# Kernel optimization log

Hardware: AMD Instinct MI355X
Metric: run time of the kernel (lower is better)

Reference implementation:

```python
import jax, jax.numpy as jnp
import numpy as np

D_MODEL = 768
D_STATE = 64
HEADDIM = 64
CHUNK = 64
EXPAND = 2
D_CONV = 4
D_INNER = EXPAND * D_MODEL          # 1536
NHEADS = D_INNER // HEADDIM         # 24
CONV_CH = D_INNER + 2 * D_STATE     # 1664
D_IN_PROJ = 2 * D_INNER + 2 * D_STATE + NHEADS  # 3224
EPS = 1e-5


def segsum(x):
    # x: (..., T) -> (..., T, T); entry [i, j] = sum_{k=j+1..i} x[k] for i>=j, -inf above diag
    T = x.shape[-1]
    cs = jnp.cumsum(x, axis=-1)
    seg = cs[..., :, None] - cs[..., None, :]
    mask = jnp.tril(jnp.ones((T, T), dtype=bool))
    return jnp.where(mask, seg, -jnp.inf)


def ssd(x, A, B, C, chunk):
    # x: (b, L, h, p), A: (b, L, h), B/C: (b, L, n)
    b, L, h, p = x.shape
    nc = L // chunk
    x = x.reshape(b, nc, chunk, h, p)
    A = A.reshape(b, nc, chunk, h).transpose(0, 3, 1, 2)   # (b, h, nc, l)
    B = B.reshape(b, nc, chunk, -1)
    C = C.reshape(b, nc, chunk, -1)
    A_cs = jnp.cumsum(A, axis=-1)                          # (b, h, nc, l)
    Lm = jnp.exp(segsum(A))                                # (b, h, nc, l, s)
    # intra-chunk (diagonal) term
    Y_diag = jnp.einsum('bcln,bcsn,bhcls,bcshp->bclhp', C, B, Lm, x)
    # per-chunk states
    decay_states = jnp.exp(A_cs[..., -1:] - A_cs)          # (b, h, nc, l)
    states = jnp.einsum('bcln,bhcl,bclhp->bchpn', B, decay_states, x)
    states = jnp.concatenate([jnp.zeros_like(states[:, :1]), states], axis=1)
    # inter-chunk recurrence via segsum over chunk totals
    chunk_sums = jnp.pad(A_cs[..., -1], ((0, 0), (0, 0), (1, 0)))
    decay_chunk = jnp.exp(segsum(chunk_sums))              # (b, h, nc+1, nc+1)
    new_states = jnp.einsum('bhzc,bchpn->bzhpn', decay_chunk, states)
    states = new_states[:, :-1]                            # (b, nc, h, p, n)
    Y_off = jnp.einsum('bcln,bchpn,bhcl->bclhp', C, states, jnp.exp(A_cs))
    return (Y_diag + Y_off).reshape(b, L, h, p)


def setup_inputs() -> dict:
    key = jax.random.key(0)
    ks = jax.random.split(key, 6)
    b, L = 2, 4096
    u = jax.random.normal(ks[0], (b, L, D_MODEL), dtype=jnp.float32)
    W_in = jax.random.normal(ks[1], (D_IN_PROJ, D_MODEL), dtype=jnp.float32) * (D_MODEL ** -0.5)
    conv_w = jax.random.normal(ks[2], (CONV_CH, 1, D_CONV), dtype=jnp.float32) * 0.3
    conv_b = jnp.zeros((CONV_CH,), dtype=jnp.float32)
    dt_bias = jnp.zeros((NHEADS,), dtype=jnp.float32)
    A_log = jax.random.normal(ks[3], (NHEADS,), dtype=jnp.float32) * 0.1
    D = jnp.ones((NHEADS,), dtype=jnp.float32)
    norm_w = jnp.ones((D_INNER,), dtype=jnp.float32)
    W_out = jax.random.normal(ks[4], (D_MODEL, D_INNER), dtype=jnp.float32) * (D_INNER ** -0.5)
    return {'u': u, 'W_in': W_in, 'conv_w': conv_w, 'conv_b': conv_b,
            'dt_bias': dt_bias, 'A_log': A_log, 'D': D, 'norm_w': norm_w, 'W_out': W_out}


def reference(u, W_in, conv_w, conv_b, dt_bias, A_log, D, norm_w, W_out):
    b, L, _ = u.shape
    zxbcdt = u @ W_in.T                                    # (b, L, d_in_proj)
    z = zxbcdt[..., :D_INNER]
    xBC = zxbcdt[..., D_INNER:D_INNER + CONV_CH]
    dt = jax.nn.softplus(zxbcdt[..., -NHEADS:] + dt_bias)  # (b, L, h)
    # causal depthwise conv (left pad d_conv-1, matches torch pad+slice)
    xBC = jax.lax.conv_general_dilated(
        xBC.transpose(0, 2, 1), conv_w, (1,), [(D_CONV - 1, 0)],
        dimension_numbers=('NCH', 'OIH', 'NCH'), feature_group_count=CONV_CH)
    xBC = jax.nn.silu(xBC.transpose(0, 2, 1) + conv_b)
    x = xBC[..., :D_INNER].reshape(b, L, NHEADS, HEADDIM)
    Bm = xBC[..., D_INNER:D_INNER + D_STATE]
    Cm = xBC[..., -D_STATE:]
    A = -jnp.exp(A_log)                                    # (h,)
    y = ssd(x * dt[..., None], A * dt, Bm, Cm, CHUNK)
    y = y + x * D[None, None, :, None]
    y = y.reshape(b, L, D_INNER)
    # gated RMSNorm
    y = y * jax.nn.silu(z)
    y = y * jax.lax.rsqrt(jnp.mean(y * y, axis=-1, keepdims=True) + EPS) * norm_w
    return y @ W_out.T
```

## Files before the change

### kernel.cpp

```cpp
#include <hip/hip_runtime.h>

typedef __attribute__((ext_vector_type(4))) float f4;
typedef __attribute__((ext_vector_type(8))) short bfx8;
typedef __attribute__((ext_vector_type(4))) float f32x4;
typedef __attribute__((ext_vector_type(4))) unsigned int u32x4;
typedef __attribute__((ext_vector_type(4))) unsigned short u16x4;
typedef __attribute__((ext_vector_type(8))) unsigned short u16x8;
typedef unsigned short ushort_t;

#define DM 768
#define DINNER 1536
#define NH 24
#define XBCW 1664
#define DINPROJ 3224
#define NPAD1 3328
#define NCHUNK 64
#define BROWS 8192
#define PADB 72

__device__ inline ushort_t f2bf(float f) {
    unsigned u = __builtin_bit_cast(unsigned, f);
    unsigned r = (u + 0x7FFF + ((u >> 16) & 1)) >> 16;
    return (ushort_t)r;
}
__device__ inline float bf2f(ushort_t u) {
    return __builtin_bit_cast(float, (unsigned)u << 16);
}
__device__ inline u32x4 pack8(f4 a, f4 b) {
    u32x4 o;
    o[0] = (unsigned)f2bf(a[0]) | ((unsigned)f2bf(a[1]) << 16);
    o[1] = (unsigned)f2bf(a[2]) | ((unsigned)f2bf(a[3]) << 16);
    o[2] = (unsigned)f2bf(b[0]) | ((unsigned)f2bf(b[1]) << 16);
    o[3] = (unsigned)f2bf(b[2]) | ((unsigned)f2bf(b[3]) << 16);
    return o;
}
__device__ inline void gl16(const void* g, void* l) {
    __builtin_amdgcn_global_load_lds((const __attribute__((address_space(1))) void*)g,
                                     (__attribute__((address_space(3))) void*)l, 16, 0, 0);
}

__global__ __launch_bounds__(256) void fill_kernel(float* out, int n, float v) {
    int i = blockIdx.x * 256 + threadIdx.x;
    if (i < n) out[i] = v;
}

__global__ __launch_bounds__(256) void cvt_kernel(const float* __restrict__ in,
                                                  ushort_t* __restrict__ outp, long n4) {
    long i = (long)blockIdx.x * 256 + threadIdx.x;
    if (i >= n4) return;
    f4 v = *(const f4*)&in[i * 4];
    u16x4 o;
    o[0] = f2bf(v[0]); o[1] = f2bf(v[1]); o[2] = f2bf(v[2]); o[3] = f2bf(v[3]);
    *(u16x4*)&outp[i * 4] = o;
}

__global__ __launch_bounds__(256) void cvt_pad_kernel(const float* __restrict__ in,
                                                      ushort_t* __restrict__ outp) {
    long q = (long)blockIdx.x * 256 + threadIdx.x;
    if (q >= (long)NPAD1 * 192) return;
    int row = (int)(q / 192);
    int cq = (int)(q % 192);
    u16x4 o = {0, 0, 0, 0};
    if (row < DINPROJ) {
        f4 v = *(const f4*)&in[(long)row * DM + cq * 4];
        o[0] = f2bf(v[0]); o[1] = f2bf(v[1]); o[2] = f2bf(v[2]); o[3] = f2bf(v[3]);
    }
    *(u16x4*)&outp[q * 4] = o;
}

template <int EPI>
__global__ __launch_bounds__(256) void gemm_bt(const ushort_t* __restrict__ A,
                                               const ushort_t* __restrict__ B,
                                               float* __restrict__ C,
                                               int K, int ldc,
                                               ushort_t* __restrict__ zbf,
                                               float* __restrict__ xbcraw,
                                               float* __restrict__ dtbT,
                                               const float* __restrict__ dt_bias) {
    __shared__ __align__(16) ushort_t As[128 * 32];
    __shared__ __align__(16) ushort_t Bs[128 * 32];
    int tid = threadIdx.x;
    int lane = tid & 63;
    int w = tid >> 6;
    int wr = w >> 1, wc = w & 1;
    int m0 = blockIdx.y * 128;
    int n0 = blockIdx.x * 128;
    int r16 = lane & 15, kg = lane >> 4;

    int row0 = tid >> 2, cof0 = (tid & 3) * 8;
    int row1 = (tid + 256) >> 2, cof1 = (tid & 3) * 8;
    const ushort_t* a0 = &A[(long)(m0 + row0) * K + cof0];
    const ushort_t* a1 = &A[(long)(m0 + row1) * K + cof1];
    const ushort_t* b0 = &B[(long)(n0 + row0) * K + cof0];
    const ushort_t* b1 = &B[(long)(n0 + row1) * K + cof1];
    char* asb = (char*)As + w * 1024;
    char* bsb = (char*)Bs + w * 1024;

    f32x4 acc[4][4] = {};

    for (int k0 = 0; k0 < K; k0 += 32) {
        gl16(a0 + k0, asb);
        gl16(a1 + k0, asb + 4096);
        gl16(b0 + k0, bsb);
        gl16(b1 + k0, bsb + 4096);
        __syncthreads();
        bfx8 af[4], bfr[4];
#pragma unroll
        for (int i = 0; i < 4; ++i) {
            af[i] = *(const bfx8*)&As[(wr * 64 + i * 16 + r16) * 32 + kg * 8];
            bfr[i] = *(const bfx8*)&Bs[(wc * 64 + i * 16 + r16) * 32 + kg * 8];
        }
#pragma unroll
        for (int i = 0; i < 4; ++i)
#pragma unroll
            for (int j = 0; j < 4; ++j)
                acc[i][j] = __builtin_amdgcn_mfma_f32_16x16x32_bf16(af[i], bfr[j], acc[i][j], 0, 0, 0);
        __syncthreads();
    }

#pragma unroll
    for (int i = 0; i < 4; ++i) {
        int rowb = m0 + wr * 64 + i * 16 + kg * 4;
#pragma unroll
        for (int j = 0; j < 4; ++j) {
            int col = n0 + wc * 64 + j * 16 + r16;
            if (EPI == 0) {
#pragma unroll
                for (int q = 0; q < 4; ++q)
                    C[(long)(rowb + q) * ldc + col] = acc[i][j][q];
            } else {
                if (n0 < DINNER) {
#pragma unroll
                    for (int q = 0; q < 4; ++q)
                        zbf[(long)(rowb + q) * DINNER + col] = f2bf(acc[i][j][q]);
                } else if (n0 < 3200) {
#pragma unroll
                    for (int q = 0; q < 4; ++q)
                        xbcraw[(long)(rowb + q) * XBCW + col - DINNER] = acc[i][j][q];
                } else if (col < DINPROJ) {
                    int h = col - 3200;
                    float bias = dt_bias[h];
#pragma unroll
                    for (int q = 0; q < 4; ++q) {
                        float v = acc[i][j][q] + bias;
                        float d = (v > 20.f) ? v : log1pf(__expf(v));
                        dtbT[(long)h * BROWS + rowb + q] = d;
                    }
                }
            }
        }
    }
}

__global__ __launch_bounds__(256) void conv_kernel(const float* __restrict__ xin,
                                                   const float* __restrict__ cw,
                                                   const float* __restrict__ cb,
                                                   float* __restrict__ xbc) {
    int ch = blockIdx.y * 256 + threadIdx.x;
    int row = blockIdx.x;
    if (ch >= XBCW) return;
    int b = row >> 12;
    int l = row & 4095;
    float acc = cb[ch];
#pragma unroll
    for (int k = 0; k < 4; ++k) {
        int ll = l - 3 + k;
        if (ll >= 0)
            acc += cw[ch * 4 + k] * xin[(long)(b * 4096 + ll) * XBCW + ch];
    }
    float s = acc / (1.f + __expf(-acc));
    xbc[(long)row * XBCW + ch] = s;
}

__global__ __launch_bounds__(256) void acs_kernel(const float* __restrict__ dtbT,
                                                  const float* __restrict__ A_log,
                                                  float* __restrict__ acs,
                                                  float* __restrict__ Tsum) {
    int bh = blockIdx.x;
    int b = bh / NH, h = bh % NH;
    int t = threadIdx.x;
    int lane = t & 63;
    float A = -__expf(A_log[h]);
    const float* dp = &dtbT[(long)h * BROWS + b * 4096];
#pragma unroll
    for (int it = 0; it < 16; ++it) {
        int c = (t >> 6) + 4 * it;
        float v = A * dp[c * 64 + lane];
#pragma unroll
        for (int off = 1; off < 64; off <<= 1) {
            float u = __shfl_up(v, off, 64);
            if (lane >= off) v += u;
        }
        acs[((long)bh * NCHUNK + c) * 64 + lane] = v;
        if (lane == 63) Tsum[bh * NCHUNK + c] = v;
    }
}

__global__ __launch_bounds__(256) void states_kernel(const float* __restrict__ xbc,
                                                     const float* __restrict__ dtbT,
                                                     const float* __restrict__ acs,
                                                     const float* __restrict__ Tsum,
                                                     ushort_t* __restrict__ states) {
    int h = blockIdx.x, c = blockIdx.y, b = blockIdx.z;
    __shared__ __align__(16) ushort_t Wt[64 * PADB];
    __shared__ __align__(16) ushort_t Bt[64 * PADB];
    int t = threadIdx.x;
    long rowg0 = (long)b * 4096 + c * 64;
    long acsb = ((long)(b * NH + h) * NCHUNK + c) * 64;
    float T = Tsum[(b * NH + h) * NCHUNK + c];
#pragma unroll
    for (int i = 0; i < 2; ++i) {
        int q = t + 256 * i;
        int l = q >> 3, sg = q & 7;
        const float* rp = &xbc[(rowg0 + l) * (long)XBCW];
        float dec = dtbT[(long)h * BROWS + rowg0 + l] * __expf(T - acs[acsb + l]);
        f4 x0 = *(const f4*)&rp[h * 64 + sg * 8];
        f4 x1 = *(const f4*)&rp[h * 64 + sg * 8 + 4];
        f4 b0 = *(const f4*)&rp[DINNER + sg * 8];
        f4 b1 = *(const f4*)&rp[DINNER + sg * 8 + 4];
#pragma unroll
        for (int jj = 0; jj < 4; ++jj) {
            Wt[(sg * 8 + jj) * PADB + l] = f2bf(x0[jj] * dec);
            Wt[(sg * 8 + 4 + jj) * PADB + l] = f2bf(x1[jj] * dec);
            Bt[(sg * 8 + jj) * PADB + l] = f2bf(b0[jj]);
            Bt[(sg * 8 + 4 + jj) * PADB + l] = f2bf(b1[jj]);
        }
    }
    __syncthreads();
    int w = t >> 6, lane = t & 63;
    int r16 = lane & 15, kg = lane >> 4;
    bfx8 aw[2];
#pragma unroll
    for (int kk = 0; kk < 2; ++kk)
        aw[kk] = *(const bfx8*)&Wt[(w * 16 + r16) * PADB + kk * 32 + kg * 8];
    f32x4 acc[4] = {};
#pragma unroll
    for (int j = 0; j < 4; ++j)
#pragma unroll
        for (int kk = 0; kk < 2; ++kk) {
            bfx8 bb = *(const bfx8*)&Bt[(j * 16 + r16) * PADB + kk * 32 + kg * 8];
            acc[j] = __builtin_amdgcn_mfma_f32_16x16x32_bf16(aw[kk], bb, acc[j], 0, 0, 0);
        }
    __syncthreads();
#pragma unroll
    for (int j = 0; j < 4; ++j)
#pragma unroll
        for (int q = 0; q < 4; ++q)
            Wt[(w * 16 + kg * 4 + q) * PADB + j * 16 + r16] = f2bf(acc[j][q]);
    __syncthreads();
    long ob = ((long)(b * NH + h) * NCHUNK + c) * 4096;
#pragma unroll
    for (int i = 0; i < 2; ++i) {
        int q = t + 256 * i;
        int p = q >> 3, sg = q & 7;
        *(u16x8*)&states[ob + p * 64 + sg * 8] = *(const u16x8*)&Wt[p * PADB + sg * 8];
    }
}

__global__ __launch_bounds__(256) void scan_kernel(const float* __restrict__ Tsum,
                                                   ushort_t* __restrict__ states) {
    int e = blockIdx.x * 256 + threadIdx.x;
    int h = blockIdx.y, b = blockIdx.z;
    long base = ((long)(b * NH + h)) * NCHUNK * 4096 + e;
    const float* Tp = &Tsum[(b * NH + h) * NCHUNK];
    float acc = 0.f;
    for (int c = 0; c < NCHUNK; ++c) {
        float cur = bf2f(states[base + (long)c * 4096]);
        states[base + (long)c * 4096] = f2bf(acc);
        acc = __expf(Tp[c]) * acc + cur;
    }
}

__global__ __launch_bounds__(256) void yfull_kernel(const float* __restrict__ xbc,
                                                    const float* __restrict__ dtbT,
                                                    const float* __restrict__ acs,
                                                    const ushort_t* __restrict__ sprev,
                                                    ushort_t* __restrict__ ybuf) {
    int h = blockIdx.x, c = blockIdx.y, b = blockIdx.z;
    __shared__ __align__(16) ushort_t Cb[64 * PADB];
    __shared__ __align__(16) ushort_t Bb[64 * PADB];
    __shared__ __align__(16) ushort_t Xt[64 * PADB];
    __shared__ __align__(16) ushort_t Sp[64 * PADB];
    __shared__ __align__(16) ushort_t Sm[64 * PADB];
    __shared__ float sAcs[64], sE[64];
    int t = threadIdx.x;
    long rowg0 = (long)b * 4096 + c * 64;
    long acsb = ((long)(b * NH + h) * NCHUNK + c) * 64;
    long spb = ((long)(b * NH + h) * NCHUNK + c) * 4096;
    if (t < 64) {
        float a = acs[acsb + t];
        sAcs[t] = a;
        sE[t] = __expf(a);
    }
#pragma unroll
    for (int i = 0; i < 2; ++i) {
        int q = t + 256 * i;
        int l = q >> 3, sg = q & 7;
        const float* rp = &xbc[(rowg0 + l) * (long)XBCW];
        f4 c0 = *(const f4*)&rp[1600 + sg * 8];
        f4 c1 = *(const f4*)&rp[1600 + sg * 8 + 4];
        *(u32x4*)&Cb[l * PADB + sg * 8] = pack8(c0, c1);
        f4 b0 = *(const f4*)&rp[DINNER + sg * 8];
        f4 b1 = *(const f4*)&rp[DINNER + sg * 8 + 4];
        *(u32x4*)&Bb[l * PADB + sg * 8] = pack8(b0, b1);
        float dtv = dtbT[(long)h * BROWS + rowg0 + l];
        f4 x0 = *(const f4*)&rp[h * 64 + sg * 8];
        f4 x1 = *(const f4*)&rp[h * 64 + sg * 8 + 4];
#pragma unroll
        for (int jj = 0; jj < 4; ++jj) {
            Xt[(sg * 8 + jj) * PADB + l] = f2bf(x0[jj] * dtv);
            Xt[(sg * 8 + 4 + jj) * PADB + l] = f2bf(x1[jj] * dtv);
        }
        *(u16x8*)&Sp[l * PADB + sg * 8] = *(const u16x8*)&sprev[spb + l * 64 + sg * 8];
    }
    __syncthreads();
    int w = t >> 6, lane = t & 63;
    int r16 = lane & 15, kg = lane >> 4;
    bfx8 ac[2];
#pragma unroll
    for (int kk = 0; kk < 2; ++kk)
        ac[kk] = *(const bfx8*)&Cb[(w * 16 + r16) * PADB + kk * 32 + kg * 8];
    f32x4 s_acc[4] = {};
#pragma unroll
    for (int j = 0; j < 4; ++j)
#pragma unroll
        for (int kk = 0; kk < 2; ++kk) {
            bfx8 bb = *(const bfx8*)&Bb[(j * 16 + r16) * PADB + kk * 32 + kg * 8];
            s_acc[j] = __builtin_amdgcn_mfma_f32_16x16x32_bf16(ac[kk], bb, s_acc[j], 0, 0, 0);
        }
#pragma unroll
    for (int j = 0; j < 4; ++j)
#pragma unroll
        for (int q = 0; q < 4; ++q) {
            int l = w * 16 + kg * 4 + q;
            int s = j * 16 + r16;
            float v = s_acc[j][q];
            v = (s <= l) ? v * __expf(sAcs[l] - sAcs[s]) : 0.f;
            Sm[l * PADB + s] = f2bf(v);
        }
    __syncthreads();
    bfx8 as[2];
#pragma unroll
    for (int kk = 0; kk < 2; ++kk)
        as[kk] = *(const bfx8*)&Sm[(w * 16 + r16) * PADB + kk * 32 + kg * 8];
    f32x4 d_acc[4] = {}, o_acc[4] = {};
#pragma unroll
    for (int j = 0; j < 4; ++j)
#pragma unroll
        for (int kk = 0; kk < 2; ++kk) {
            bfx8 xb = *(const bfx8*)&Xt[(j * 16 + r16) * PADB + kk * 32 + kg * 8];
            d_acc[j] = __builtin_amdgcn_mfma_f32_16x16x32_bf16(as[kk], xb, d_acc[j], 0, 0, 0);
            bfx8 sb = *(const bfx8*)&Sp[(j * 16 + r16) * PADB + kk * 32 + kg * 8];
            o_acc[j] = __builtin_amdgcn_mfma_f32_16x16x32_bf16(ac[kk], sb, o_acc[j], 0, 0, 0);
        }
#pragma unroll
    for (int j = 0; j < 4; ++j)
#pragma unroll
        for (int q = 0; q < 4; ++q) {
            int l = w * 16 + kg * 4 + q;
            int p = j * 16 + r16;
            Bb[l * PADB + p] = f2bf(d_acc[j][q] + sE[l] * o_acc[j][q]);
        }
    __syncthreads();
#pragma unroll
    for (int i = 0; i < 2; ++i) {
        int q = t + 256 * i;
        int l = q >> 3, sg = q & 7;
        *(u16x8*)&ybuf[(rowg0 + l) * (long)DINNER + h * 64 + sg * 8] =
            *(const u16x8*)&Bb[l * PADB + sg * 8];
    }
}

__global__ __launch_bounds__(256) void norm_kernel(const ushort_t* __restrict__ ybuf,
                                                   const float* __restrict__ xbc,
                                                   const ushort_t* __restrict__ zbf,
                                                   const float* __restrict__ Dp,
                                                   const float* __restrict__ normw,
                                                   ushort_t* __restrict__ ybf) {
    int row = blockIdx.x;
    int t = threadIdx.x;
    float g[6];
    float ss = 0.f;
#pragma unroll
    for (int i = 0; i < 6; ++i) {
        int j = t + 256 * i;
        int h = j >> 6;
        float x = xbc[(long)row * XBCW + j];
        float yy = bf2f(ybuf[(long)row * DINNER + j]) + x * Dp[h];
        float z = bf2f(zbf[(long)row * DINNER + j]);
        float gz = z / (1.f + __expf(-z));
        float v = yy * gz;
        g[i] = v;
        ss += v * v;
    }
#pragma unroll
    for (int o = 32; o > 0; o >>= 1) ss += __shfl_xor(ss, o, 64);
    __shared__ float wsum[4];
    __shared__ float sscale;
    int w = t >> 6;
    if ((t & 63) == 0) wsum[w] = ss;
    __syncthreads();
    if (t == 0) {
        float tot = wsum[0] + wsum[1] + wsum[2] + wsum[3];
        sscale = rsqrtf(tot / (float)DINNER + 1e-5f);
    }
    __syncthreads();
    float sc = sscale;
#pragma unroll
    for (int i = 0; i < 6; ++i) {
        int j = t + 256 * i;
        ybf[(long)row * DINNER + j] = f2bf(g[i] * sc * normw[j]);
    }
}

extern "C" void kernel_launch(void* const* d_in, const int* in_sizes, int n_in,
                              void* d_out, int out_size, void* d_ws, size_t ws_size,
                              hipStream_t stream) {
    const float* u = (const float*)d_in[0];
    const float* W_in = (const float*)d_in[1];
    const float* conv_w = (const float*)d_in[2];
    const float* conv_b = (const float*)d_in[3];
    const float* dt_bias = (const float*)d_in[4];
    const float* A_log = (const float*)d_in[5];
    const float* Dp = (const float*)d_in[6];
    const float* norm_w = (const float*)d_in[7];
    const float* W_out = (const float*)d_in[8];
    float* out = (float*)d_out;

    char* ws = (char*)d_ws;
    size_t off = 0;
    auto alloc = [&](size_t bytes) {
        void* p = ws + off;
        off += (bytes + 255) & ~(size_t)255;
        return p;
    };
    ushort_t* zbf = (ushort_t*)alloc((size_t)BROWS * DINNER * 2);
    float* xbcraw = (float*)alloc((size_t)BROWS * XBCW * 4);
    float* xbc = (float*)alloc((size_t)BROWS * XBCW * 4);
    float* dtbT = (float*)alloc((size_t)NH * BROWS * 4);
    float* acs = (float*)alloc((size_t)2 * NH * NCHUNK * 64 * 4);
    float* Tsum = (float*)alloc((size_t)2 * NH * NCHUNK * 4);
    ushort_t* states = (ushort_t*)alloc((size_t)2 * NH * NCHUNK * 4096 * 2);
    ushort_t* ybuf = (ushort_t*)alloc((size_t)BROWS * DINNER * 2);
    ushort_t* ybf = (ushort_t*)xbcraw;
    ushort_t* ubf = ybuf;
    ushort_t* winbf = states;
    ushort_t* woutbf = states;

    if (off > ws_size) {
        fill_kernel<<<(out_size + 255) / 256, 256, 0, stream>>>(out, out_size, 12345.0f);
        return;
    }

    cvt_kernel<<<(BROWS * DM / 4 + 255) / 256, 256, 0, stream>>>(u, ubf, (long)BROWS * DM / 4);
    cvt_pad_kernel<<<((long)NPAD1 * 192 + 255) / 256, 256, 0, stream>>>(W_in, winbf);

    gemm_bt<1><<<dim3(26, 64), 256, 0, stream>>>(ubf, winbf, nullptr, DM, 0,
                                                 zbf, xbcraw, dtbT, dt_bias);

    conv_kernel<<<dim3(BROWS, 7), 256, 0, stream>>>(xbcraw, conv_w, conv_b, xbc);

    acs_kernel<<<2 * NH, 256, 0, stream>>>(dtbT, A_log, acs, Tsum);
    states_kernel<<<dim3(NH, NCHUNK, 2), 256, 0, stream>>>(xbc, dtbT, acs, Tsum, states);
    scan_kernel<<<dim3(16, NH, 2), 256, 0, stream>>>(Tsum, states);
    yfull_kernel<<<dim3(NH, NCHUNK, 2), 256, 0, stream>>>(xbc, dtbT, acs, states, ybuf);

    norm_kernel<<<BROWS, 256, 0, stream>>>(ybuf, xbc, zbf, Dp, norm_w, ybf);

    cvt_kernel<<<(DM * DINNER / 4 + 255) / 256, 256, 0, stream>>>(W_out, woutbf, (long)DM * DINNER / 4);
    gemm_bt<0><<<dim3(6, 64), 256, 0, stream>>>(ybf, woutbf, out, DINNER, DM,
                                                nullptr, nullptr, nullptr, nullptr);
}
```

Measured before the change: 291.5 us.

## Double-buffer GEMM LDS tiles and store conv output as bf16

The bf16 GEMM now keeps two LDS buffers, so the global-to-LDS load for the next K tile is issued while the current tile's MFMAs run, with one barrier per iteration. Separately, the conv+SiLU output xBC is stored as bf16 instead of fp32, which halves its write and read traffic in the states, yfull and norm kernels and removes per-element fp32-to-bf16 packing there. The extra rounding of x for the D skip term in norm is a small accuracy risk, and the larger LDS footprint may lower GEMM occupancy.

```diff
diff --git a/kernel.cpp b/kernel.cpp
--- a/kernel.cpp
+++ b/kernel.cpp
@@ -25,14 +25,6 @@
 }
 __device__ inline float bf2f(ushort_t u) {
     return __builtin_bit_cast(float, (unsigned)u << 16);
-}
-__device__ inline u32x4 pack8(f4 a, f4 b) {
-    u32x4 o;
-    o[0] = (unsigned)f2bf(a[0]) | ((unsigned)f2bf(a[1]) << 16);
-    o[1] = (unsigned)f2bf(a[2]) | ((unsigned)f2bf(a[3]) << 16);
-    o[2] = (unsigned)f2bf(b[0]) | ((unsigned)f2bf(b[1]) << 16);
-    o[3] = (unsigned)f2bf(b[2]) | ((unsigned)f2bf(b[3]) << 16);
-    return o;
 }
 __device__ inline void gl16(const void* g, void* l) {
     __builtin_amdgcn_global_load_lds((const __attribute__((address_space(1))) void*)g,
@@ -77,8 +69,8 @@
                                                float* __restrict__ xbcraw,
                                                float* __restrict__ dtbT,
                                                const float* __restrict__ dt_bias) {
-    __shared__ __align__(16) ushort_t As[128 * 32];
-    __shared__ __align__(16) ushort_t Bs[128 * 32];
+    __shared__ __align__(16) ushort_t As[2][128 * 32];
+    __shared__ __align__(16) ushort_t Bs[2][128 * 32];
     int tid = threadIdx.x;
     int lane = tid & 63;
     int w = tid >> 6;
@@ -88,34 +80,44 @@
     int r16 = lane & 15, kg = lane >> 4;
 
     int row0 = tid >> 2, cof0 = (tid & 3) * 8;
-    int row1 = (tid + 256) >> 2, cof1 = (tid & 3) * 8;
     const ushort_t* a0 = &A[(long)(m0 + row0) * K + cof0];
-    const ushort_t* a1 = &A[(long)(m0 + row1) * K + cof1];
+    const ushort_t* a1 = &A[(long)(m0 + row0 + 64) * K + cof0];
     const ushort_t* b0 = &B[(long)(n0 + row0) * K + cof0];
-    const ushort_t* b1 = &B[(long)(n0 + row1) * K + cof1];
-    char* asb = (char*)As + w * 1024;
-    char* bsb = (char*)Bs + w * 1024;
+    const ushort_t* b1 = &B[(long)(n0 + row0 + 64) * K + cof0];
+    char* asb[2] = {(char*)&As[0][0] + w * 1024, (char*)&As[1][0] + w * 1024};
+    char* bsb[2] = {(char*)&Bs[0][0] + w * 1024, (char*)&Bs[1][0] + w * 1024};
 
     f32x4 acc[4][4] = {};
 
-    for (int k0 = 0; k0 < K; k0 += 32) {
-        gl16(a0 + k0, asb);
-        gl16(a1 + k0, asb + 4096);
-        gl16(b0 + k0, bsb);
-        gl16(b1 + k0, bsb + 4096);
-        __syncthreads();
+    gl16(a0, asb[0]); gl16(a1, asb[0] + 4096);
+    gl16(b0, bsb[0]); gl16(b1, bsb[0] + 4096);
+    asm volatile("s_waitcnt vmcnt(0)" ::: "memory");
+    __builtin_amdgcn_s_barrier();
+
+    int nk = K >> 5;
+    for (int t = 0; t < nk; ++t) {
+        int cur = t & 1;
+        if (t + 1 < nk) {
+            int k1 = (t + 1) << 5;
+            gl16(a0 + k1, asb[cur ^ 1]); gl16(a1 + k1, asb[cur ^ 1] + 4096);
+            gl16(b0 + k1, bsb[cur ^ 1]); gl16(b1 + k1, bsb[cur ^ 1] + 4096);
+        }
+        const ushort_t* Asc = &As[cur][0];
+        const ushort_t* Bsc = &Bs[cur][0];
         bfx8 af[4], bfr[4];
 #pragma unroll
         for (int i = 0; i < 4; ++i) {
-            af[i] = *(const bfx8*)&As[(wr * 64 + i * 16 + r16) * 32 + kg * 8];
-            bfr[i] = *(const bfx8*)&Bs[(wc * 64 + i * 16 + r16) * 32 + kg * 8];
+            af[i] = *(const bfx8*)&Asc[(wr * 64 + i * 16 + r16) * 32 + kg * 8];
+            bfr[i] = *(const bfx8*)&Bsc[(wc * 64 + i * 16 + r16) * 32 + kg * 8];
         }
 #pragma unroll
         for (int i = 0; i < 4; ++i)
 #pragma unroll
             for (int j = 0; j < 4; ++j)
                 acc[i][j] = __builtin_amdgcn_mfma_f32_16x16x32_bf16(af[i], bfr[j], acc[i][j], 0, 0, 0);
-        __syncthreads();
+        asm volatile("s_waitcnt vmcnt(0) lgkmcnt(0)" ::: "memory");
+        __builtin_amdgcn_sched_barrier(0);
+        __builtin_amdgcn_s_barrier();
     }
 
 #pragma unroll
@@ -155,7 +157,7 @@
 __global__ __launch_bounds__(256) void conv_kernel(const float* __restrict__ xin,
                                                    const float* __restrict__ cw,
                                                    const float* __restrict__ cb,
-                                                   float* __restrict__ xbc) {
+                                                   ushort_t* __restrict__ xbc) {
     int ch = blockIdx.y * 256 + threadIdx.x;
     int row = blockIdx.x;
     if (ch >= XBCW) return;
@@ -169,7 +171,7 @@
             acc += cw[ch * 4 + k] * xin[(long)(b * 4096 + ll) * XBCW + ch];
     }
     float s = acc / (1.f + __expf(-acc));
-    xbc[(long)row * XBCW + ch] = s;
+    xbc[(long)row * XBCW + ch] = f2bf(s);
 }
 
 __global__ __launch_bounds__(256) void acs_kernel(const float* __restrict__ dtbT,
@@ -196,7 +198,7 @@
     }
 }
 
-__global__ __launch_bounds__(256) void states_kernel(const float* __restrict__ xbc,
+__global__ __launch_bounds__(256) void states_kernel(const ushort_t* __restrict__ xbc,
                                                      const float* __restrict__ dtbT,
                                                      const float* __restrict__ acs,
                                                      const float* __restrict__ Tsum,
@@ -212,18 +214,14 @@
     for (int i = 0; i < 2; ++i) {
         int q = t + 256 * i;
         int l = q >> 3, sg = q & 7;
-        const float* rp = &xbc[(rowg0 + l) * (long)XBCW];
+        const ushort_t* rp = &xbc[(rowg0 + l) * (long)XBCW];
         float dec = dtbT[(long)h * BROWS + rowg0 + l] * __expf(T - acs[acsb + l]);
-        f4 x0 = *(const f4*)&rp[h * 64 + sg * 8];
-        f4 x1 = *(const f4*)&rp[h * 64 + sg * 8 + 4];
-        f4 b0 = *(const f4*)&rp[DINNER + sg * 8];
-        f4 b1 = *(const f4*)&rp[DINNER + sg * 8 + 4];
-#pragma unroll
-        for (int jj = 0; jj < 4; ++jj) {
-            Wt[(sg * 8 + jj) * PADB + l] = f2bf(x0[jj] * dec);
-            Wt[(sg * 8 + 4 + jj) * PADB + l] = f2bf(x1[jj] * dec);
-            Bt[(sg * 8 + jj) * PADB + l] = f2bf(b0[jj]);
-            Bt[(sg * 8 + 4 + jj) * PADB + l] = f2bf(b1[jj]);
+        u16x8 xv = *(const u16x8*)&rp[h * 64 + sg * 8];
+        u16x8 bv = *(const u16x8*)&rp[DINNER + sg * 8];
+#pragma unroll
+        for (int jj = 0; jj < 8; ++jj) {
+            Wt[(sg * 8 + jj) * PADB + l] = f2bf(bf2f(xv[jj]) * dec);
+            Bt[(sg * 8 + jj) * PADB + l] = bv[jj];
         }
     }
     __syncthreads();
@@ -271,7 +269,7 @@
     }
 }
 
-__global__ __launch_bounds__(256) void yfull_kernel(const float* __restrict__ xbc,
+__global__ __launch_bounds__(256) void yfull_kernel(const ushort_t* __restrict__ xbc,
                                                     const float* __restrict__ dtbT,
                                                     const float* __restrict__ acs,
                                                     const ushort_t* __restrict__ sprev,
@@ -296,21 +294,14 @@
     for (int i = 0; i < 2; ++i) {
         int q = t + 256 * i;
         int l = q >> 3, sg = q & 7;
-        const float* rp = &xbc[(rowg0 + l) * (long)XBCW];
-        f4 c0 = *(const f4*)&rp[1600 + sg * 8];
-        f4 c1 = *(const f4*)&rp[1600 + sg * 8 + 4];
-        *(u32x4*)&Cb[l * PADB + sg * 8] = pack8(c0, c1);
-        f4 b0 = *(const f4*)&rp[DINNER + sg * 8];
-        f4 b1 = *(const f4*)&rp[DINNER + sg * 8 + 4];
-        *(u32x4*)&Bb[l * PADB + sg * 8] = pack8(b0, b1);
+        const ushort_t* rp = &xbc[(rowg0 + l) * (long)XBCW];
+        *(u16x8*)&Cb[l * PADB + sg * 8] = *(const u16x8*)&rp[1600 + sg * 8];
+        *(u16x8*)&Bb[l * PADB + sg * 8] = *(const u16x8*)&rp[DINNER + sg * 8];
         float dtv = dtbT[(long)h * BROWS + rowg0 + l];
-        f4 x0 = *(const f4*)&rp[h * 64 + sg * 8];
-        f4 x1 = *(const f4*)&rp[h * 64 + sg * 8 + 4];
-#pragma unroll
-        for (int jj = 0; jj < 4; ++jj) {
-            Xt[(sg * 8 + jj) * PADB + l] = f2bf(x0[jj] * dtv);
-            Xt[(sg * 8 + 4 + jj) * PADB + l] = f2bf(x1[jj] * dtv);
-        }
+        u16x8 xv = *(const u16x8*)&rp[h * 64 + sg * 8];
+#pragma unroll
+        for (int jj = 0; jj < 8; ++jj)
+            Xt[(sg * 8 + jj) * PADB + l] = f2bf(bf2f(xv[jj]) * dtv);
         *(u16x8*)&Sp[l * PADB + sg * 8] = *(const u16x8*)&sprev[spb + l * 64 + sg * 8];
     }
     __syncthreads();
@@ -372,7 +363,7 @@
 }
 
 __global__ __launch_bounds__(256) void norm_kernel(const ushort_t* __restrict__ ybuf,
-                                                   const float* __restrict__ xbc,
+                                                   const ushort_t* __restrict__ xbc,
                                                    const ushort_t* __restrict__ zbf,
                                                    const float* __restrict__ Dp,
                                                    const float* __restrict__ normw,
@@ -385,7 +376,7 @@
     for (int i = 0; i < 6; ++i) {
         int j = t + 256 * i;
         int h = j >> 6;
-        float x = xbc[(long)row * XBCW + j];
+        float x = bf2f(xbc[(long)row * XBCW + j]);
         float yy = bf2f(ybuf[(long)row * DINNER + j]) + x * Dp[h];
         float z = bf2f(zbf[(long)row * DINNER + j]);
         float gz = z / (1.f + __expf(-z));
@@ -436,7 +427,7 @@
     };
     ushort_t* zbf = (ushort_t*)alloc((size_t)BROWS * DINNER * 2);
     float* xbcraw = (float*)alloc((size_t)BROWS * XBCW * 4);
-    float* xbc = (float*)alloc((size_t)BROWS * XBCW * 4);
+    ushort_t* xbc = (ushort_t*)alloc((size_t)BROWS * XBCW * 2);
     float* dtbT = (float*)alloc((size_t)NH * BROWS * 4);
     float* acs = (float*)alloc((size_t)2 * NH * NCHUNK * 64 * 4);
     float* Tsum = (float*)alloc((size_t)2 * NH * NCHUNK * 4);
```

Measured after the change: 280.2 us. 3.9% less time.
